# Kernel optimization log

Measured on AMD Instinct MI355X. Metric: run time of the kernel, lower is better.

Reference implementation:

```python
import jax, jax.numpy as jnp
import numpy as np

N = 100000      # nodes
E = 1600000     # edges (avg degree 16)
F_IN = 15       # num_features from source
H1, H2, OUT = 64, 32, 2
BN_EPS = 1e-5


def _lin(key, out_dim, in_dim):
    return (jax.random.normal(key, (out_dim, in_dim), dtype=jnp.float32)
            * np.float32(1.0 / np.sqrt(in_dim)))


def setup_inputs() -> dict:
    key = jax.random.key(0)
    ks = jax.random.split(key, 16)
    x = jax.random.normal(ks[0], (N, F_IN), dtype=jnp.float32)
    edge_index = jax.random.randint(ks[1], (2, E), 0, N)
    return {
        "x": x,
        "edge_index": edge_index,
        # SAGEConv layer 1 (lin_l on aggregated neighbors w/ bias, lin_r on root no bias)
        "W1l": _lin(ks[2], H1, F_IN), "b1l": jnp.zeros((H1,), jnp.float32),
        "W1r": _lin(ks[3], H1, F_IN),
        "g1": jnp.ones((H1,), jnp.float32), "beta1": jnp.zeros((H1,), jnp.float32),
        # SAGEConv layer 2
        "W2l": _lin(ks[4], H2, H1), "b2l": jnp.zeros((H2,), jnp.float32),
        "W2r": _lin(ks[5], H2, H1),
        "g2": jnp.ones((H2,), jnp.float32), "beta2": jnp.zeros((H2,), jnp.float32),
        # SAGEConv layer 3
        "W3l": _lin(ks[6], OUT, H2), "b3l": jnp.zeros((OUT,), jnp.float32),
        "W3r": _lin(ks[7], OUT, H2),
    }


def sage_conv(x, src, dst, Wl, bl, Wr, n):
    # mean-aggregate neighbor features x[src] at dst, then linear + root linear
    msg = x[src]                                           # [E, d]
    agg = jax.ops.segment_sum(msg, dst, num_segments=n)    # [N, d]
    deg = jax.ops.segment_sum(jnp.ones((src.shape[0],), x.dtype), dst,
                              num_segments=n)              # [N]
    mean = agg / jnp.maximum(deg, 1.0)[:, None]
    return mean @ Wl.T + bl + x @ Wr.T


def batch_norm(x, gamma, beta):
    mu = x.mean(axis=0)
    var = x.var(axis=0)  # biased, as torch BN uses for normalization
    return (x - mu) * jax.lax.rsqrt(var + BN_EPS) * gamma + beta


def reference(x, edge_index, W1l, b1l, W1r, g1, beta1,
              W2l, b2l, W2r, g2, beta2, W3l, b3l, W3r):
    src, dst = edge_index[0], edge_index[1]
    n = x.shape[0]
    h = sage_conv(x, src, dst, W1l, b1l, W1r, n)
    h = jax.nn.relu(batch_norm(h, g1, beta1))
    h = sage_conv(h, src, dst, W2l, b2l, W2r, n)
    h = jax.nn.relu(batch_norm(h, g2, beta2))
    h = sage_conv(h, src, dst, W3l, b3l, W3r, n)
    return jax.nn.log_softmax(h, axis=1)
```

## Files before the change

kernel.cpp:

```cpp
#include <hip/hip_runtime.h>
#include <hip/hip_bf16.h>
#include <math.h>

#define N_NODES 100000
#define N_EDGES 1600000
#define F_IN 15
#define H1 64
#define H2 32
#define BN_EPS 1e-5f
#define NBLK 2048
#define RELU1(v) fmaxf(fmaf((v), scale, shift), 0.f)


__global__ void k_deg(const int* __restrict__ dst, int* __restrict__ deg) {
    int e = blockIdx.x * blockDim.x + threadIdx.x;
    if (e < N_EDGES) atomicAdd(&deg[dst[e]], 1);
}

__global__ void k_scan_a(const int* __restrict__ deg, int* __restrict__ off,
                         int* __restrict__ part) {
    __shared__ int s[1024];
    int i = blockIdx.x * 1024 + threadIdx.x;
    int v = (i < N_NODES) ? deg[i] : 0;
    s[threadIdx.x] = v;
    __syncthreads();
    for (int o = 1; o < 1024; o <<= 1) {
        int t = (threadIdx.x >= o) ? s[threadIdx.x - o] : 0;
        __syncthreads();
        s[threadIdx.x] += t;
        __syncthreads();
    }
    if (i < N_NODES) off[i] = s[threadIdx.x] - v;
    if (threadIdx.x == 1023) part[blockIdx.x] = s[1023];
}

__global__ void k_scan_b(int* __restrict__ part, int nb) {
    __shared__ int s[128];
    int v = (threadIdx.x < nb) ? part[threadIdx.x] : 0;
    s[threadIdx.x] = v;
    __syncthreads();
    for (int o = 1; o < 128; o <<= 1) {
        int t = (threadIdx.x >= o) ? s[threadIdx.x - o] : 0;
        __syncthreads();
        s[threadIdx.x] += t;
        __syncthreads();
    }
    if (threadIdx.x < nb) part[threadIdx.x] = s[threadIdx.x] - v;
}

__global__ void k_scan_c(int* __restrict__ off, int* __restrict__ cur,
                         const int* __restrict__ part) {
    int i = blockIdx.x * blockDim.x + threadIdx.x;
    if (i < N_NODES) {
        int v = off[i] + part[i >> 10];
        off[i] = v;
        cur[i] = v;
    }
    if (i == 0) off[N_NODES] = N_EDGES;
}

__global__ void k_fill(const int* __restrict__ src, const int* __restrict__ dst,
                       int* __restrict__ cur, int* __restrict__ srt) {
    int e = blockIdx.x * blockDim.x + threadIdx.x;
    if (e < N_EDGES) {
        int p = atomicAdd(&cur[dst[e]], 1);
        srt[p] = src[e];
    }
}


__launch_bounds__(256)
__global__ void k_l1(const float* __restrict__ x, const int* __restrict__ off,
                     const int* __restrict__ srt,
                     const float* __restrict__ W1l, const float* __restrict__ b1l,
                     const float* __restrict__ W1r,
                     float* __restrict__ h1, float* __restrict__ stats) {
    __shared__ float m_lds[4][16], o_lds[4][16];
    __shared__ float sred[2 * H1];
    int lane = threadIdx.x & 63;
    int w = threadIdx.x >> 6;
    int gw = blockIdx.x * 4 + w;
    const int NW = NBLK * 4;

    float wl[F_IN], wr[F_IN];
#pragma unroll
    for (int k = 0; k < F_IN; ++k) {
        wl[k] = W1l[lane * F_IN + k];
        wr[k] = W1r[lane * F_IN + k];
    }
    float bj = b1l[lane];

    if (threadIdx.x < 2 * H1) sred[threadIdx.x] = 0.f;
    __syncthreads();

    float sS = 0.f, sQ = 0.f;
    for (int n = gw; n < N_NODES; n += NW) {
        int o0 = off[n], o1 = off[n + 1];
        float sum = 0.f;
        int i = o0;
        for (; i + 8 <= o1; i += 8) {
            int s0 = srt[i+0], s1 = srt[i+1], s2 = srt[i+2], s3 = srt[i+3],
                s4 = srt[i+4], s5 = srt[i+5], s6 = srt[i+6], s7 = srt[i+7];
            if (lane < F_IN) {
                float v0 = x[(long)s0*F_IN+lane], v1 = x[(long)s1*F_IN+lane],
                      v2 = x[(long)s2*F_IN+lane], v3 = x[(long)s3*F_IN+lane],
                      v4 = x[(long)s4*F_IN+lane], v5 = x[(long)s5*F_IN+lane],
                      v6 = x[(long)s6*F_IN+lane], v7 = x[(long)s7*F_IN+lane];
                sum += ((v0+v1)+(v2+v3)) + ((v4+v5)+(v6+v7));
            }
        }
        for (; i < o1; ++i) {
            int s = srt[i];
            if (lane < F_IN) sum += x[(long)s*F_IN+lane];
        }
        float inv = 1.f / (float)max(o1 - o0, 1);
        if (lane < F_IN) {
            m_lds[w][lane] = sum * inv;
            o_lds[w][lane] = x[(long)n*F_IN+lane];
        }
        float acc = bj;
#pragma unroll
        for (int k = 0; k < F_IN; ++k)
            acc += m_lds[w][k] * wl[k] + o_lds[w][k] * wr[k];
        h1[(long)n*H1 + lane] = acc;
        sS += acc; sQ += acc * acc;
    }
    atomicAdd(&sred[lane], sS);
    atomicAdd(&sred[H1 + lane], sQ);
    __syncthreads();
    if (threadIdx.x < 2 * H1) atomicAdd(&stats[threadIdx.x], sred[threadIdx.x]);
}


__launch_bounds__(256)
__global__ void k_l2(const float* __restrict__ h1, const int* __restrict__ off,
                     const int* __restrict__ srt,
                     const float* __restrict__ W2l, const float* __restrict__ b2l,
                     const float* __restrict__ W2r,
                     const float* __restrict__ g1, const float* __restrict__ beta1,
                     const float* __restrict__ stats1,
                     float* __restrict__ h2, float* __restrict__ stats2) {
    __shared__ float meanb[4][H1], ownb[4][H1];
    __shared__ float sred[2 * H2];
    int lane = threadIdx.x & 63;
    int w = threadIdx.x >> 6;
    int gw = blockIdx.x * 4 + w;
    const int NW = NBLK * 4;

    float mu = stats1[lane] * (1.f / N_NODES);
    float var = stats1[H1 + lane] * (1.f / N_NODES) - mu * mu;
    float scale = rsqrtf(var + BN_EPS) * g1[lane];
    float shift = beta1[lane] - mu * scale;

    float wcol[H1];
    const float* wsrc = (lane < H2) ? (W2l + lane * H1) : (W2r + (lane - H2) * H1);
#pragma unroll
    for (int k = 0; k < H1; ++k) wcol[k] = wsrc[k];
    float bj = (lane < H2) ? b2l[lane] : 0.f;

    if (threadIdx.x < 2 * H2) sred[threadIdx.x] = 0.f;
    __syncthreads();

    float sS = 0.f, sQ = 0.f;
    for (int n = gw; n < N_NODES; n += NW) {
        int o0 = off[n], o1 = off[n + 1];
        float sum = 0.f;
        int i = o0;
        for (; i + 8 <= o1; i += 8) {
            int s0 = srt[i+0], s1 = srt[i+1], s2 = srt[i+2], s3 = srt[i+3],
                s4 = srt[i+4], s5 = srt[i+5], s6 = srt[i+6], s7 = srt[i+7];
            float v0 = h1[(long)s0*H1+lane], v1 = h1[(long)s1*H1+lane],
                  v2 = h1[(long)s2*H1+lane], v3 = h1[(long)s3*H1+lane],
                  v4 = h1[(long)s4*H1+lane], v5 = h1[(long)s5*H1+lane],
                  v6 = h1[(long)s6*H1+lane], v7 = h1[(long)s7*H1+lane];
            sum += ((RELU1(v0)+RELU1(v1)) + (RELU1(v2)+RELU1(v3)))
                 + ((RELU1(v4)+RELU1(v5)) + (RELU1(v6)+RELU1(v7)));
        }
        for (; i < o1; ++i) {
            int s = srt[i];
            sum += RELU1(h1[(long)s*H1+lane]);
        }
        float inv = 1.f / (float)max(o1 - o0, 1);
        meanb[w][lane] = sum * inv;
        ownb[w][lane] = RELU1(h1[(long)n*H1+lane]);

        const float* bsel = (lane < H2) ? &meanb[w][0] : &ownb[w][0];
        float acc = bj;
#pragma unroll
        for (int k = 0; k < H1; ++k) acc += bsel[k] * wcol[k];
        float other = __shfl_xor(acc, 32, 64);
        if (lane < H2) {
            float hp = acc + other;
            h2[(long)n*H2 + lane] = hp;
            sS += hp; sQ += hp * hp;
        }
    }
    if (lane < H2) {
        atomicAdd(&sred[lane], sS);
        atomicAdd(&sred[H2 + lane], sQ);
    }
    __syncthreads();
    if (threadIdx.x < 2 * H2) atomicAdd(&stats2[threadIdx.x], sred[threadIdx.x]);
}


__launch_bounds__(256)
__global__ void k_l3(const float* __restrict__ h2, const int* __restrict__ off,
                     const int* __restrict__ srt,
                     const float* __restrict__ W3l, const float* __restrict__ b3l,
                     const float* __restrict__ W3r,
                     const float* __restrict__ g2, const float* __restrict__ beta2,
                     const float* __restrict__ stats2, float* __restrict__ out) {
    int lane = threadIdx.x & 63;
    int w = threadIdx.x >> 6;
    int h = lane >> 5;
    int j = lane & 31;
    int gw = blockIdx.x * 4 + w;
    const int NW = NBLK * 4;

    float mu = stats2[j] * (1.f / N_NODES);
    float var = stats2[H2 + j] * (1.f / N_NODES) - mu * mu;
    float scale = rsqrtf(var + BN_EPS) * g2[j];
    float shift = beta2[j] - mu * scale;

    float wl0 = W3l[j], wl1 = W3l[H2 + j];
    float wr0 = W3r[j], wr1 = W3r[H2 + j];
    float b0 = b3l[0], b1 = b3l[1];

    for (int p = gw; p < N_NODES / 2; p += NW) {
        int n = p * 2 + h;
        int o0 = off[n], o1 = off[n + 1];
        float sum = 0.f;
        int i = o0;
        for (; i + 8 <= o1; i += 8) {
            int s0 = srt[i+0], s1 = srt[i+1], s2 = srt[i+2], s3 = srt[i+3],
                s4 = srt[i+4], s5 = srt[i+5], s6 = srt[i+6], s7 = srt[i+7];
            float v0 = h2[(long)s0*H2+j], v1 = h2[(long)s1*H2+j],
                  v2 = h2[(long)s2*H2+j], v3 = h2[(long)s3*H2+j],
                  v4 = h2[(long)s4*H2+j], v5 = h2[(long)s5*H2+j],
                  v6 = h2[(long)s6*H2+j], v7 = h2[(long)s7*H2+j];
            sum += ((RELU1(v0)+RELU1(v1)) + (RELU1(v2)+RELU1(v3)))
                 + ((RELU1(v4)+RELU1(v5)) + (RELU1(v6)+RELU1(v7)));
        }
        for (; i < o1; ++i) {
            int s = srt[i];
            sum += RELU1(h2[(long)s*H2+j]);
        }
        float inv = 1.f / (float)max(o1 - o0, 1);
        float meanj = sum * inv;
        float ownj = RELU1(h2[(long)n*H2+j]);
        float p0 = meanj * wl0 + ownj * wr0;
        float p1 = meanj * wl1 + ownj * wr1;
#pragma unroll
        for (int s = 16; s > 0; s >>= 1) {
            p0 += __shfl_xor(p0, s, 32);
            p1 += __shfl_xor(p1, s, 32);
        }
        if (j == 0) {
            float z0 = p0 + b0, z1 = p1 + b1;
            float m = fmaxf(z0, z1);
            float l = m + logf(__expf(z0 - m) + __expf(z1 - m));
            out[(long)n * 2 + 0] = z0 - l;
            out[(long)n * 2 + 1] = z1 - l;
        }
    }
}


extern "C" void kernel_launch(void* const* d_in, const int* in_sizes, int n_in,
                              void* d_out, int out_size, void* d_ws, size_t ws_size,
                              hipStream_t stream) {
    const float* x    = (const float*)d_in[0];
    const int*   ei   = (const int*)d_in[1];
    const float* W1l  = (const float*)d_in[2];
    const float* b1l  = (const float*)d_in[3];
    const float* W1r  = (const float*)d_in[4];
    const float* g1   = (const float*)d_in[5];
    const float* bt1  = (const float*)d_in[6];
    const float* W2l  = (const float*)d_in[7];
    const float* b2l  = (const float*)d_in[8];
    const float* W2r  = (const float*)d_in[9];
    const float* g2   = (const float*)d_in[10];
    const float* bt2  = (const float*)d_in[11];
    const float* W3l  = (const float*)d_in[12];
    const float* b3l  = (const float*)d_in[13];
    const float* W3r  = (const float*)d_in[14];
    float* out = (float*)d_out;

    float* stats1 = (float*)d_ws;
    float* stats2 = stats1 + 128;
    int* deg  = (int*)d_ws + 256;
    int* off  = deg + 100096;
    int* cur  = off + 100096;
    int* srt  = cur + 100096;
    int* part = srt + 1600000;
    float* h1 = (float*)(part + 256);
    float* h2 = h1 + (size_t)N_NODES * H1;

    const int* srcv = ei;
    const int* dstv = ei + N_EDGES;

    hipMemsetAsync(d_ws, 0, (256 + 100096) * sizeof(int), stream);

    k_deg   <<<(N_EDGES + 255) / 256, 256, 0, stream>>>(dstv, deg);
    k_scan_a<<<98, 1024, 0, stream>>>(deg, off, part);
    k_scan_b<<<1, 128, 0, stream>>>(part, 98);
    k_scan_c<<<(N_NODES + 255) / 256, 256, 0, stream>>>(off, cur, part);
    k_fill  <<<(N_EDGES + 255) / 256, 256, 0, stream>>>(srcv, dstv, cur, srt);
    k_l1    <<<NBLK, 256, 0, stream>>>(x, off, srt, W1l, b1l, W1r, h1, stats1);
    k_l2    <<<NBLK, 256, 0, stream>>>(h1, off, srt, W2l, b2l, W2r, g1, bt1, stats1, h2, stats2);
    k_l3    <<<NBLK, 256, 0, stream>>>(h2, off, srt, W3l, b3l, W3r, g2, bt2, stats2, out);
}
```

Baseline: 603.3 us.

## Store intermediate activations as bf16 and batch neighbor index loads via shuffles

Hidden activations h1 and h2 are now stored as bf16 instead of fp32, which halves the bytes moved by the gather-heavy aggregation in layers 2 and 3. The gather loops gain a 16-wide unrolled stage, and in layers 1 and 2 one coalesced load of neighbor indices is broadcast to all lanes by wavefront shuffles. Layer 2 keeps its weights in padded LDS instead of 64 registers per thread, trading register pressure for LDS reads. BN statistics are still accumulated in fp32, but the rounding to bf16 reduces accuracy of the stored activations.

```diff
diff --git a/kernel.cpp b/kernel.cpp
--- a/kernel.cpp
+++ b/kernel.cpp
@@ -11,6 +11,15 @@
 #define NBLK 2048
 #define RELU1(v) fmaxf(fmaf((v), scale, shift), 0.f)
 
+__device__ __forceinline__ unsigned short f2bf(float f) {
+    unsigned u = __float_as_uint(f);
+    u += 0x7FFFu + ((u >> 16) & 1u);
+    return (unsigned short)(u >> 16);
+}
+__device__ __forceinline__ float bf2f(unsigned short h) {
+    return __uint_as_float(((unsigned)h) << 16);
+}
+
 
 __global__ void k_deg(const int* __restrict__ dst, int* __restrict__ deg) {
     int e = blockIdx.x * blockDim.x + threadIdx.x;
@@ -74,7 +83,7 @@
                      const int* __restrict__ srt,
                      const float* __restrict__ W1l, const float* __restrict__ b1l,
                      const float* __restrict__ W1r,
-                     float* __restrict__ h1, float* __restrict__ stats) {
+                     unsigned short* __restrict__ h1b, float* __restrict__ stats) {
     __shared__ float m_lds[4][16], o_lds[4][16];
     __shared__ float sred[2 * H1];
     int lane = threadIdx.x & 63;
@@ -98,31 +107,42 @@
         int o0 = off[n], o1 = off[n + 1];
         float sum = 0.f;
         int i = o0;
+        for (; i + 16 <= o1; i += 16) {
+            int my = (lane < 16) ? srt[i + lane] : 0;
+            float v[16];
+#pragma unroll
+            for (int b = 0; b < 16; ++b) {
+                int s = __shfl(my, b, 64);
+                v[b] = (lane < F_IN) ? x[(long)s * F_IN + lane] : 0.f;
+            }
+#pragma unroll
+            for (int b = 0; b < 16; ++b) sum += v[b];
+        }
         for (; i + 8 <= o1; i += 8) {
-            int s0 = srt[i+0], s1 = srt[i+1], s2 = srt[i+2], s3 = srt[i+3],
-                s4 = srt[i+4], s5 = srt[i+5], s6 = srt[i+6], s7 = srt[i+7];
-            if (lane < F_IN) {
-                float v0 = x[(long)s0*F_IN+lane], v1 = x[(long)s1*F_IN+lane],
-                      v2 = x[(long)s2*F_IN+lane], v3 = x[(long)s3*F_IN+lane],
-                      v4 = x[(long)s4*F_IN+lane], v5 = x[(long)s5*F_IN+lane],
-                      v6 = x[(long)s6*F_IN+lane], v7 = x[(long)s7*F_IN+lane];
-                sum += ((v0+v1)+(v2+v3)) + ((v4+v5)+(v6+v7));
+            int my = (lane < 8) ? srt[i + lane] : 0;
+            float v[8];
+#pragma unroll
+            for (int b = 0; b < 8; ++b) {
+                int s = __shfl(my, b, 64);
+                v[b] = (lane < F_IN) ? x[(long)s * F_IN + lane] : 0.f;
             }
+#pragma unroll
+            for (int b = 0; b < 8; ++b) sum += v[b];
         }
         for (; i < o1; ++i) {
             int s = srt[i];
-            if (lane < F_IN) sum += x[(long)s*F_IN+lane];
+            if (lane < F_IN) sum += x[(long)s * F_IN + lane];
         }
         float inv = 1.f / (float)max(o1 - o0, 1);
         if (lane < F_IN) {
             m_lds[w][lane] = sum * inv;
-            o_lds[w][lane] = x[(long)n*F_IN+lane];
+            o_lds[w][lane] = x[(long)n * F_IN + lane];
         }
         float acc = bj;
 #pragma unroll
         for (int k = 0; k < F_IN; ++k)
             acc += m_lds[w][k] * wl[k] + o_lds[w][k] * wr[k];
-        h1[(long)n*H1 + lane] = acc;
+        h1b[(long)n * H1 + lane] = f2bf(acc);
         sS += acc; sQ += acc * acc;
     }
     atomicAdd(&sred[lane], sS);
@@ -133,13 +153,14 @@
 
 
 __launch_bounds__(256)
-__global__ void k_l2(const float* __restrict__ h1, const int* __restrict__ off,
+__global__ void k_l2(const unsigned short* __restrict__ h1b, const int* __restrict__ off,
                      const int* __restrict__ srt,
                      const float* __restrict__ W2l, const float* __restrict__ b2l,
                      const float* __restrict__ W2r,
                      const float* __restrict__ g1, const float* __restrict__ beta1,
                      const float* __restrict__ stats1,
-                     float* __restrict__ h2, float* __restrict__ stats2) {
+                     unsigned short* __restrict__ h2b, float* __restrict__ stats2) {
+    __shared__ float wlds[H1][H1 + 1];
     __shared__ float meanb[4][H1], ownb[4][H1];
     __shared__ float sred[2 * H2];
     int lane = threadIdx.x & 63;
@@ -152,12 +173,11 @@
     float scale = rsqrtf(var + BN_EPS) * g1[lane];
     float shift = beta1[lane] - mu * scale;
 
-    float wcol[H1];
-    const float* wsrc = (lane < H2) ? (W2l + lane * H1) : (W2r + (lane - H2) * H1);
-#pragma unroll
-    for (int k = 0; k < H1; ++k) wcol[k] = wsrc[k];
+    for (int idx = threadIdx.x; idx < H1 * H1; idx += 256) {
+        int jj = idx >> 6, kk = idx & 63;
+        wlds[jj][kk] = (jj < H2) ? W2l[jj * H1 + kk] : W2r[(jj - H2) * H1 + kk];
+    }
     float bj = (lane < H2) ? b2l[lane] : 0.f;
-
     if (threadIdx.x < 2 * H2) sred[threadIdx.x] = 0.f;
     __syncthreads();
 
@@ -166,32 +186,44 @@
         int o0 = off[n], o1 = off[n + 1];
         float sum = 0.f;
         int i = o0;
+        for (; i + 16 <= o1; i += 16) {
+            int my = (lane < 16) ? srt[i + lane] : 0;
+            float v[16];
+#pragma unroll
+            for (int b = 0; b < 16; ++b) {
+                int s = __shfl(my, b, 64);
+                v[b] = bf2f(h1b[(long)s * H1 + lane]);
+            }
+#pragma unroll
+            for (int b = 0; b < 16; ++b) sum += RELU1(v[b]);
+        }
         for (; i + 8 <= o1; i += 8) {
-            int s0 = srt[i+0], s1 = srt[i+1], s2 = srt[i+2], s3 = srt[i+3],
-                s4 = srt[i+4], s5 = srt[i+5], s6 = srt[i+6], s7 = srt[i+7];
-            float v0 = h1[(long)s0*H1+lane], v1 = h1[(long)s1*H1+lane],
-                  v2 = h1[(long)s2*H1+lane], v3 = h1[(long)s3*H1+lane],
-                  v4 = h1[(long)s4*H1+lane], v5 = h1[(long)s5*H1+lane],
-                  v6 = h1[(long)s6*H1+lane], v7 = h1[(long)s7*H1+lane];
-            sum += ((RELU1(v0)+RELU1(v1)) + (RELU1(v2)+RELU1(v3)))
-                 + ((RELU1(v4)+RELU1(v5)) + (RELU1(v6)+RELU1(v7)));
+            int my = (lane < 8) ? srt[i + lane] : 0;
+            float v[8];
+#pragma unroll
+            for (int b = 0; b < 8; ++b) {
+                int s = __shfl(my, b, 64);
+                v[b] = bf2f(h1b[(long)s * H1 + lane]);
+            }
+#pragma unroll
+            for (int b = 0; b < 8; ++b) sum += RELU1(v[b]);
         }
         for (; i < o1; ++i) {
             int s = srt[i];
-            sum += RELU1(h1[(long)s*H1+lane]);
+            sum += RELU1(bf2f(h1b[(long)s * H1 + lane]));
         }
         float inv = 1.f / (float)max(o1 - o0, 1);
         meanb[w][lane] = sum * inv;
-        ownb[w][lane] = RELU1(h1[(long)n*H1+lane]);
+        ownb[w][lane] = RELU1(bf2f(h1b[(long)n * H1 + lane]));
 
         const float* bsel = (lane < H2) ? &meanb[w][0] : &ownb[w][0];
         float acc = bj;
 #pragma unroll
-        for (int k = 0; k < H1; ++k) acc += bsel[k] * wcol[k];
+        for (int k = 0; k < H1; ++k) acc += bsel[k] * wlds[lane][k];
         float other = __shfl_xor(acc, 32, 64);
         if (lane < H2) {
             float hp = acc + other;
-            h2[(long)n*H2 + lane] = hp;
+            h2b[(long)n * H2 + lane] = f2bf(hp);
             sS += hp; sQ += hp * hp;
         }
     }
@@ -205,7 +237,7 @@
 
 
 __launch_bounds__(256)
-__global__ void k_l3(const float* __restrict__ h2, const int* __restrict__ off,
+__global__ void k_l3(const unsigned short* __restrict__ h2b, const int* __restrict__ off,
                      const int* __restrict__ srt,
                      const float* __restrict__ W3l, const float* __restrict__ b3l,
                      const float* __restrict__ W3r,
@@ -232,23 +264,33 @@
         int o0 = off[n], o1 = off[n + 1];
         float sum = 0.f;
         int i = o0;
+        for (; i + 16 <= o1; i += 16) {
+            int sidx[16];
+#pragma unroll
+            for (int b = 0; b < 16; ++b) sidx[b] = srt[i + b];
+            float v[16];
+#pragma unroll
+            for (int b = 0; b < 16; ++b) v[b] = bf2f(h2b[(long)sidx[b] * H2 + j]);
+#pragma unroll
+            for (int b = 0; b < 16; ++b) sum += RELU1(v[b]);
+        }
         for (; i + 8 <= o1; i += 8) {
-            int s0 = srt[i+0], s1 = srt[i+1], s2 = srt[i+2], s3 = srt[i+3],
-                s4 = srt[i+4], s5 = srt[i+5], s6 = srt[i+6], s7 = srt[i+7];
-            float v0 = h2[(long)s0*H2+j], v1 = h2[(long)s1*H2+j],
-                  v2 = h2[(long)s2*H2+j], v3 = h2[(long)s3*H2+j],
-                  v4 = h2[(long)s4*H2+j], v5 = h2[(long)s5*H2+j],
-                  v6 = h2[(long)s6*H2+j], v7 = h2[(long)s7*H2+j];
-            sum += ((RELU1(v0)+RELU1(v1)) + (RELU1(v2)+RELU1(v3)))
-                 + ((RELU1(v4)+RELU1(v5)) + (RELU1(v6)+RELU1(v7)));
+            int sidx[8];
+#pragma unroll
+            for (int b = 0; b < 8; ++b) sidx[b] = srt[i + b];
+            float v[8];
+#pragma unroll
+            for (int b = 0; b < 8; ++b) v[b] = bf2f(h2b[(long)sidx[b] * H2 + j]);
+#pragma unroll
+            for (int b = 0; b < 8; ++b) sum += RELU1(v[b]);
         }
         for (; i < o1; ++i) {
             int s = srt[i];
-            sum += RELU1(h2[(long)s*H2+j]);
+            sum += RELU1(bf2f(h2b[(long)s * H2 + j]));
         }
         float inv = 1.f / (float)max(o1 - o0, 1);
         float meanj = sum * inv;
-        float ownj = RELU1(h2[(long)n*H2+j]);
+        float ownj = RELU1(bf2f(h2b[(long)n * H2 + j]));
         float p0 = meanj * wl0 + ownj * wr0;
         float p1 = meanj * wl1 + ownj * wr1;
 #pragma unroll
@@ -294,8 +336,8 @@
     int* cur  = off + 100096;
     int* srt  = cur + 100096;
     int* part = srt + 1600000;
-    float* h1 = (float*)(part + 256);
-    float* h2 = h1 + (size_t)N_NODES * H1;
+    unsigned short* h1b = (unsigned short*)(part + 256);
+    unsigned short* h2b = h1b + (size_t)N_NODES * H1;
 
     const int* srcv = ei;
     const int* dstv = ei + N_EDGES;
@@ -307,7 +349,7 @@
     k_scan_b<<<1, 128, 0, stream>>>(part, 98);
     k_scan_c<<<(N_NODES + 255) / 256, 256, 0, stream>>>(off, cur, part);
     k_fill  <<<(N_EDGES + 255) / 256, 256, 0, stream>>>(srcv, dstv, cur, srt);
-    k_l1    <<<NBLK, 256, 0, stream>>>(x, off, srt, W1l, b1l, W1r, h1, stats1);
-    k_l2    <<<NBLK, 256, 0, stream>>>(h1, off, srt, W2l, b2l, W2r, g1, bt1, stats1, h2, stats2);
-    k_l3    <<<NBLK, 256, 0, stream>>>(h2, off, srt, W3l, b3l, W3r, g2, bt2, stats2, out);
-}
+    k_l1    <<<NBLK, 256, 0, stream>>>(x, off, srt, W1l, b1l, W1r, h1b, stats1);
+    k_l2    <<<NBLK, 256, 0, stream>>>(h1b, off, srt, W2l, b2l, W2r, g1, bt1, stats1, h2b, stats2);
+    k_l3    <<<NBLK, 256, 0, stream>>>(h2b, off, srt, W3l, b3l, W3r, g2, bt2, stats2, out);
+}
```

Result: slower. 637.8 us (+5.7%).
